# Kernel tuning notes

Measured on AMD Instinct MI355X. Metric: run time of the kernel, lower is better.

The kernel has to match this reference:

```python
import jax, jax.numpy as jnp
import numpy as np

N_NODES = 100000
N_EDGES = 600000
N_GRAPHS = 256
HID = 128
IN_DIM = 7
POCKET_DIM = 28
BN_EPS = 1e-5


def setup_inputs() -> dict:
    key = jax.random.key(0)
    ks = jax.random.split(key, 24)
    d = {}
    d['x'] = jax.random.normal(ks[0], (N_NODES, IN_DIM), dtype=jnp.float32)
    d['edge_index'] = jax.random.randint(ks[1], (2, N_EDGES), 0, N_NODES, dtype=jnp.int32)
    d['batch'] = jnp.sort(jax.random.randint(ks[2], (N_NODES,), 0, N_GRAPHS, dtype=jnp.int32))
    d['pocket'] = jax.random.normal(ks[3], (POCKET_DIM,), dtype=jnp.float32)
    # GCN layer weights (PyG GCNConv: lin then normalized aggregation, bias after)
    def glorot(k, shape):
        lim = np.sqrt(6.0 / (shape[0] + shape[1]))
        return jax.random.uniform(k, shape, jnp.float32, -lim, lim)
    d['W0'] = glorot(ks[4], (IN_DIM, HID)); d['b0'] = jnp.zeros((HID,), jnp.float32)
    d['W1'] = glorot(ks[5], (HID, HID)); d['b1'] = jnp.zeros((HID,), jnp.float32)
    d['W2'] = glorot(ks[6], (HID, HID)); d['b2'] = jnp.zeros((HID,), jnp.float32)
    # BatchNorm (eval mode) params for 3 layers
    d['bn_gamma'] = jax.random.uniform(ks[7], (3, HID), jnp.float32, 0.5, 1.5)
    d['bn_beta'] = 0.1 * jax.random.normal(ks[8], (3, HID), dtype=jnp.float32)
    d['bn_mean'] = 0.1 * jax.random.normal(ks[9], (3, HID), dtype=jnp.float32)
    d['bn_var'] = jax.random.uniform(ks[10], (3, HID), jnp.float32, 0.5, 1.5)
    # pocket MLP: 28 -> 64 -> 64
    d['pw1'] = glorot(ks[11], (POCKET_DIM, 64)); d['pb1'] = jnp.zeros((64,), jnp.float32)
    d['pw2'] = glorot(ks[12], (64, 64)); d['pb2'] = jnp.zeros((64,), jnp.float32)
    # classifier: 192 -> 96 -> 1
    d['cw1'] = glorot(ks[13], (HID + 64, 96)); d['cb1'] = jnp.zeros((96,), jnp.float32)
    d['cw2'] = glorot(ks[14], (96, 1)); d['cb2'] = jnp.zeros((1,), jnp.float32)
    return d


def reference(x, edge_index, batch, pocket, W0, b0, W1, b1, W2, b2,
              bn_gamma, bn_beta, bn_mean, bn_var,
              pw1, pb1, pw2, pb2, cw1, cb1, cw2, cb2):
    src, dst = edge_index[0], edge_index[1]
    n = x.shape[0]
    # degree with self-loops (GCNConv default add_self_loops=True)
    deg = jax.ops.segment_sum(jnp.ones((src.shape[0],), x.dtype), dst, num_segments=n) + 1.0
    dinv = jax.lax.rsqrt(deg)                      # [N]
    norm = dinv[src] * dinv[dst]                   # [E] edge normalization
    self_norm = (dinv * dinv)[:, None]             # [N,1] self-loop norm

    h = x
    for i, (W, b) in enumerate(((W0, b0), (W1, b1), (W2, b2))):
        hl = h @ W                                  # [N,HID]
        agg = jax.ops.segment_sum(hl[src] * norm[:, None], dst, num_segments=n)
        agg = agg + hl * self_norm + b
        # BatchNorm1d in eval mode with running stats
        bn = (agg - bn_mean[i]) * (bn_gamma[i] * jax.lax.rsqrt(bn_var[i] + BN_EPS)) + bn_beta[i]
        h = jax.nn.relu(bn)                         # dropout is identity in eval

    # global mean pool over graphs
    sums = jax.ops.segment_sum(h, batch, num_segments=N_GRAPHS)          # [B,HID]
    cnts = jax.ops.segment_sum(jnp.ones((n,), h.dtype), batch, num_segments=N_GRAPHS)
    lig = sums / jnp.maximum(cnts, 1.0)[:, None]

    # pocket MLP, broadcast to batch
    p = jax.nn.relu(pocket @ pw1 + pb1) @ pw2 + pb2                      # [64]
    pe = jnp.broadcast_to(p[None, :], (N_GRAPHS, 64))

    emb = jnp.concatenate([lig, pe], axis=1)                             # [B,192]
    logits = (jax.nn.relu(emb @ cw1 + cb1) @ cw2 + cb2)[:, 0]            # [B]
    return logits
```

## Files before the change

### kernel.cpp

```cpp
#include <hip/hip_runtime.h>

#define NN 100000
#define NE 600000
#define NG 256
#define HID 128
#define BN_EPS 1e-5f

#define SCAN_TILE 1024
#define NTILES ((NN + SCAN_TILE - 1) / SCAN_TILE)
#define MM_TILES (NN / 32)

typedef __attribute__((ext_vector_type(8))) short short8;
typedef __attribute__((ext_vector_type(4))) float float4v;

__device__ __forceinline__ unsigned short f2bf_rn(float f) {
    unsigned u = __float_as_uint(f);
    unsigned r = u + 0x7FFFu + ((u >> 16) & 1u);
    return (unsigned short)(r >> 16);
}
__device__ __forceinline__ float bf2f(unsigned short h) {
    return __uint_as_float((unsigned)h << 16);
}
__device__ __forceinline__ void unpack8(uint4 u, float* f) {
    f[0] = __uint_as_float(u.x << 16); f[1] = __uint_as_float(u.x & 0xFFFF0000u);
    f[2] = __uint_as_float(u.y << 16); f[3] = __uint_as_float(u.y & 0xFFFF0000u);
    f[4] = __uint_as_float(u.z << 16); f[5] = __uint_as_float(u.z & 0xFFFF0000u);
    f[6] = __uint_as_float(u.w << 16); f[7] = __uint_as_float(u.w & 0xFFFF0000u);
}


__global__ __launch_bounds__(256) void hist_kernel(const int* __restrict__ dst, int* __restrict__ cnt) {
    int e = blockIdx.x * blockDim.x + threadIdx.x;
    if (e < NE) atomicAdd(&cnt[dst[e]], 1);
}


__global__ __launch_bounds__(256) void scan_a(const int* __restrict__ cnt, int* __restrict__ rs,
                                              int* __restrict__ tsum, float* __restrict__ dinv) {
    __shared__ int s[256];
    int t = threadIdx.x;
    int base = blockIdx.x * SCAN_TILE;
    int idx = base + t * 4;
    int v0 = (idx + 0 < NN) ? cnt[idx + 0] : 0;
    int v1 = (idx + 1 < NN) ? cnt[idx + 1] : 0;
    int v2 = (idx + 2 < NN) ? cnt[idx + 2] : 0;
    int v3 = (idx + 3 < NN) ? cnt[idx + 3] : 0;
    if (idx + 0 < NN) dinv[idx + 0] = rsqrtf((float)v0 + 1.0f);
    if (idx + 1 < NN) dinv[idx + 1] = rsqrtf((float)v1 + 1.0f);
    if (idx + 2 < NN) dinv[idx + 2] = rsqrtf((float)v2 + 1.0f);
    if (idx + 3 < NN) dinv[idx + 3] = rsqrtf((float)v3 + 1.0f);
    int local = v0 + v1 + v2 + v3;
    s[t] = local;
    __syncthreads();
    for (int off = 1; off < 256; off <<= 1) {
        int x = (t >= off) ? s[t - off] : 0;
        __syncthreads();
        s[t] += x;
        __syncthreads();
    }
    int pre = s[t] - local;
    if (t == 255) tsum[blockIdx.x] = s[255];
    if (idx + 0 < NN) rs[idx + 0] = pre; pre += v0;
    if (idx + 1 < NN) rs[idx + 1] = pre; pre += v1;
    if (idx + 2 < NN) rs[idx + 2] = pre; pre += v2;
    if (idx + 3 < NN) rs[idx + 3] = pre;
}

__global__ __launch_bounds__(128) void scan_b(int* __restrict__ tsum) {
    __shared__ int s[128];
    int t = threadIdx.x;
    int v = (t < NTILES) ? tsum[t] : 0;
    s[t] = v;
    __syncthreads();
    for (int off = 1; off < 128; off <<= 1) {
        int x = (t >= off) ? s[t - off] : 0;
        __syncthreads();
        s[t] += x;
        __syncthreads();
    }
    if (t < NTILES) tsum[t] = s[t] - v;
}

__global__ __launch_bounds__(256) void scan_c(int* __restrict__ rs, const int* __restrict__ tsum,
                                              int* __restrict__ cursor) {
    int t = threadIdx.x;
    int base = blockIdx.x * SCAN_TILE;
    int off = tsum[blockIdx.x];
    for (int k = 0; k < 4; k++) {
        int idx = base + t * 4 + k;
        if (idx < NN) {
            int v = rs[idx] + off;
            rs[idx] = v;
            cursor[idx] = v;
        }
    }
    if (blockIdx.x == 0 && t == 0) rs[NN] = NE;
}


__global__ __launch_bounds__(256) void bucket_kernel(const int* __restrict__ src, const int* __restrict__ dst,
                                                     int* __restrict__ cursor, int* __restrict__ esrc) {
    int e = blockIdx.x * blockDim.x + threadIdx.x;
    if (e < NE) {
        int pos = atomicAdd(&cursor[dst[e]], 1);
        esrc[pos] = src[e];
    }
}


__global__ __launch_bounds__(256) void prep_kernel(const float* __restrict__ W1, const float* __restrict__ W2,
                                                   unsigned short* __restrict__ w1hi, unsigned short* __restrict__ w1lo,
                                                   unsigned short* __restrict__ w2hi, unsigned short* __restrict__ w2lo,
                                                   const float* __restrict__ pocket,
                                                   const float* __restrict__ pw1, const float* __restrict__ pb1,
                                                   const float* __restrict__ pw2, const float* __restrict__ pb2,
                                                   float* __restrict__ pv) {
    if (blockIdx.x < 64) {
        int t = blockIdx.x * 256 + threadIdx.x;
        int k = t >> 7, n = t & 127;
        int to = n * HID + k;
        float v1 = W1[t];
        unsigned short h1 = f2bf_rn(v1);
        w1hi[to] = h1;
        w1lo[to] = f2bf_rn(v1 - bf2f(h1));
        float v2 = W2[t];
        unsigned short h2 = f2bf_rn(v2);
        w2hi[to] = h2;
        w2lo[to] = f2bf_rn(v2 - bf2f(h2));
    } else {
        __shared__ float t1[64];
        int j = threadIdx.x;
        if (j < 64) {
            float acc = pb1[j];
            for (int k = 0; k < 28; k++) acc = fmaf(pocket[k], pw1[k * 64 + j], acc);
            t1[j] = fmaxf(acc, 0.f);
        }
        __syncthreads();
        if (j < 64) {
            float acc2 = pb2[j];
            for (int k = 0; k < 64; k++) acc2 = fmaf(t1[k], pw2[k * 64 + j], acc2);
            pv[j] = acc2;
        }
    }
}


__global__ __launch_bounds__(256) void xagg_kernel(const float* __restrict__ x,
                                                   const int* __restrict__ rs,
                                                   const int* __restrict__ esrc,
                                                   const float* __restrict__ dinv,
                                                   float* __restrict__ xa) {
    int t = blockIdx.x * blockDim.x + threadIdx.x;
    int f = t & 7;
    int n = t >> 3;
    if (n >= NN) return;
    float acc = 0.f;
    if (f < 7) {
        float di = dinv[n];
        acc = x[n * 7 + f] * di * di;
        int e0 = rs[n], e1 = rs[n + 1];
        int e = e0;
        for (; e + 1 < e1; e += 2) {
            int s0 = esrc[e], s1 = esrc[e + 1];
            float w0 = dinv[s0] * di, w1 = dinv[s1] * di;
            float a0 = x[s0 * 7 + f];
            float a1 = x[s1 * 7 + f];
            acc = fmaf(a0, w0, acc);
            acc = fmaf(a1, w1, acc);
        }
        if (e < e1) {
            int s0 = esrc[e];
            acc = fmaf(x[s0 * 7 + f], dinv[s0] * di, acc);
        }
    }
    xa[n * 8 + f] = acc;
}


__global__ __launch_bounds__(256) void l0_transform(const float* __restrict__ xa,
                                                    const float* __restrict__ W,
                                                    const float* __restrict__ b,
                                                    const float* __restrict__ gamma,
                                                    const float* __restrict__ beta,
                                                    const float* __restrict__ mean,
                                                    const float* __restrict__ var,
                                                    unsigned short* __restrict__ ohi) {
    int c4 = threadIdx.x & 31;
    int r  = threadIdx.x >> 5;
    float w[7][4];
#pragma unroll
    for (int k = 0; k < 7; k++)
#pragma unroll
        for (int i = 0; i < 4; i++) w[k][i] = W[k * HID + c4 * 4 + i];
    float4 bb = ((const float4*)b)[c4];
    float4 ga = ((const float4*)gamma)[c4];
    float4 be = ((const float4*)beta)[c4];
    float4 me = ((const float4*)mean)[c4];
    float4 va = ((const float4*)var)[c4];
    float4 sc;
    sc.x = ga.x * rsqrtf(va.x + BN_EPS);
    sc.y = ga.y * rsqrtf(va.y + BN_EPS);
    sc.z = ga.z * rsqrtf(va.z + BN_EPS);
    sc.w = ga.w * rsqrtf(va.w + BN_EPS);
    __shared__ float s[8][8];
    for (int n0 = blockIdx.x * 8; n0 < NN; n0 += gridDim.x * 8) {
        __syncthreads();
        if (threadIdx.x < 64) s[threadIdx.x >> 3][threadIdx.x & 7] = xa[n0 * 8 + threadIdx.x];
        __syncthreads();
        float o0 = bb.x, o1 = bb.y, o2 = bb.z, o3 = bb.w;
#pragma unroll
        for (int k = 0; k < 7; k++) {
            float xv = s[r][k];
            o0 = fmaf(xv, w[k][0], o0);
            o1 = fmaf(xv, w[k][1], o1);
            o2 = fmaf(xv, w[k][2], o2);
            o3 = fmaf(xv, w[k][3], o3);
        }
        ushort4 hi4;
        hi4.x = f2bf_rn(fmaxf(fmaf(o0 - me.x, sc.x, be.x), 0.f));
        hi4.y = f2bf_rn(fmaxf(fmaf(o1 - me.y, sc.y, be.y), 0.f));
        hi4.z = f2bf_rn(fmaxf(fmaf(o2 - me.z, sc.z, be.z), 0.f));
        hi4.w = f2bf_rn(fmaxf(fmaf(o3 - me.w, sc.w, be.w), 0.f));
        *(ushort4*)(ohi + (size_t)(n0 + r) * HID + c4 * 4) = hi4;
    }
}


__global__ __launch_bounds__(256) void mm_mfma(const unsigned short* __restrict__ A,
                                               const unsigned short* __restrict__ Whi,
                                               const unsigned short* __restrict__ Wlo,
                                               unsigned short* __restrict__ out) {
    int wave = threadIdx.x >> 6;
    int lane = threadIdx.x & 63;
    int mrow = lane & 15;
    int quad = lane >> 4;
    int n0 = wave * 32;

    short8 bh[2][4], bl[2][4];
#pragma unroll
    for (int ct = 0; ct < 2; ct++) {
#pragma unroll
        for (int kc = 0; kc < 4; kc++) {
            size_t off = (size_t)(n0 + ct * 16 + mrow) * HID + kc * 32 + quad * 8;
            bh[ct][kc] = *(const short8*)(Whi + off);
            bl[ct][kc] = *(const short8*)(Wlo + off);
        }
    }

    int tile = blockIdx.x;
    if (tile >= MM_TILES) return;

    short8 ah[2][4];
#pragma unroll
    for (int rt = 0; rt < 2; rt++)
#pragma unroll
        for (int kc = 0; kc < 4; kc++)
            ah[rt][kc] = *(const short8*)(A + (size_t)(tile * 32 + rt * 16 + mrow) * HID + kc * 32 + quad * 8);

    for (;;) {
        int nt = tile + gridDim.x;
        bool has_next = nt < MM_TILES;
        short8 an[2][4];
        if (has_next) {
#pragma unroll
            for (int rt = 0; rt < 2; rt++)
#pragma unroll
                for (int kc = 0; kc < 4; kc++)
                    an[rt][kc] = *(const short8*)(A + (size_t)(nt * 32 + rt * 16 + mrow) * HID + kc * 32 + quad * 8);
        }

        float4v acc[2][2];
#pragma unroll
        for (int rt = 0; rt < 2; rt++)
#pragma unroll
            for (int ct = 0; ct < 2; ct++) {
                acc[rt][ct].x = 0.f; acc[rt][ct].y = 0.f;
                acc[rt][ct].z = 0.f; acc[rt][ct].w = 0.f;
            }

#pragma unroll
        for (int kc = 0; kc < 4; kc++)
#pragma unroll
            for (int rt = 0; rt < 2; rt++)
#pragma unroll
                for (int ct = 0; ct < 2; ct++) {
                    acc[rt][ct] = __builtin_amdgcn_mfma_f32_16x16x32_bf16(ah[rt][kc], bh[ct][kc], acc[rt][ct], 0, 0, 0);
                    acc[rt][ct] = __builtin_amdgcn_mfma_f32_16x16x32_bf16(ah[rt][kc], bl[ct][kc], acc[rt][ct], 0, 0, 0);
                }

        int m0 = tile * 32;
#pragma unroll
        for (int rt = 0; rt < 2; rt++)
#pragma unroll
            for (int ct = 0; ct < 2; ct++) {
                int col = n0 + ct * 16 + mrow;
#pragma unroll
                for (int r = 0; r < 4; r++) {
                    int row = m0 + rt * 16 + quad * 4 + r;
                    out[(size_t)row * HID + col] = f2bf_rn(acc[rt][ct][r]);
                }
            }

        if (!has_next) break;
#pragma unroll
        for (int rt = 0; rt < 2; rt++)
#pragma unroll
            for (int kc = 0; kc < 4; kc++) ah[rt][kc] = an[rt][kc];
        tile = nt;
    }
}


__global__ __launch_bounds__(256) void gather_bn(const unsigned short* __restrict__ hl,
                                                 const int* __restrict__ rs,
                                                 const int* __restrict__ esrc,
                                                 const float* __restrict__ dinv,
                                                 const float* __restrict__ b,
                                                 const float* __restrict__ gamma,
                                                 const float* __restrict__ beta,
                                                 const float* __restrict__ mean,
                                                 const float* __restrict__ var,
                                                 unsigned short* __restrict__ ohi) {
    int t = blockIdx.x * blockDim.x + threadIdx.x;
    int lane = t & 15;
    int n = t >> 4;
    if (n >= NN) return;
    const uint4* hlv = (const uint4*)hl;
    float di = dinv[n];
    float dsq = di * di;

    float acc[8], v[8];
    {
        uint4 sv = hlv[(size_t)n * 16 + lane];
        unpack8(sv, v);
        float4 bA = ((const float4*)b)[lane * 2];
        float4 bB = ((const float4*)b)[lane * 2 + 1];
        acc[0] = fmaf(v[0], dsq, bA.x); acc[1] = fmaf(v[1], dsq, bA.y);
        acc[2] = fmaf(v[2], dsq, bA.z); acc[3] = fmaf(v[3], dsq, bA.w);
        acc[4] = fmaf(v[4], dsq, bB.x); acc[5] = fmaf(v[5], dsq, bB.y);
        acc[6] = fmaf(v[6], dsq, bB.z); acc[7] = fmaf(v[7], dsq, bB.w);
    }

    int e0 = rs[n], e1 = rs[n + 1];
    int e = e0;
    for (; e + 3 < e1; e += 4) {
        int s0 = esrc[e], s1 = esrc[e + 1], s2 = esrc[e + 2], s3 = esrc[e + 3];
        float w0 = dinv[s0] * di, w1 = dinv[s1] * di;
        float w2 = dinv[s2] * di, w3 = dinv[s3] * di;
        uint4 u0 = hlv[(size_t)s0 * 16 + lane];
        uint4 u1 = hlv[(size_t)s1 * 16 + lane];
        uint4 u2 = hlv[(size_t)s2 * 16 + lane];
        uint4 u3 = hlv[(size_t)s3 * 16 + lane];
        unpack8(u0, v);
#pragma unroll
        for (int i = 0; i < 8; i++) acc[i] = fmaf(v[i], w0, acc[i]);
        unpack8(u1, v);
#pragma unroll
        for (int i = 0; i < 8; i++) acc[i] = fmaf(v[i], w1, acc[i]);
        unpack8(u2, v);
#pragma unroll
        for (int i = 0; i < 8; i++) acc[i] = fmaf(v[i], w2, acc[i]);
        unpack8(u3, v);
#pragma unroll
        for (int i = 0; i < 8; i++) acc[i] = fmaf(v[i], w3, acc[i]);
    }
    for (; e < e1; e++) {
        int s0 = esrc[e];
        float w0 = dinv[s0] * di;
        uint4 u0 = hlv[(size_t)s0 * 16 + lane];
        unpack8(u0, v);
#pragma unroll
        for (int i = 0; i < 8; i++) acc[i] = fmaf(v[i], w0, acc[i]);
    }

    float4 gA = ((const float4*)gamma)[lane * 2], gB = ((const float4*)gamma)[lane * 2 + 1];
    float4 eA = ((const float4*)beta)[lane * 2],  eB = ((const float4*)beta)[lane * 2 + 1];
    float4 mA = ((const float4*)mean)[lane * 2],  mB = ((const float4*)mean)[lane * 2 + 1];
    float4 vA = ((const float4*)var)[lane * 2],   vB = ((const float4*)var)[lane * 2 + 1];
    float o[8];
    o[0] = fmaxf(fmaf(acc[0] - mA.x, gA.x * rsqrtf(vA.x + BN_EPS), eA.x), 0.f);
    o[1] = fmaxf(fmaf(acc[1] - mA.y, gA.y * rsqrtf(vA.y + BN_EPS), eA.y), 0.f);
    o[2] = fmaxf(fmaf(acc[2] - mA.z, gA.z * rsqrtf(vA.z + BN_EPS), eA.z), 0.f);
    o[3] = fmaxf(fmaf(acc[3] - mA.w, gA.w * rsqrtf(vA.w + BN_EPS), eA.w), 0.f);
    o[4] = fmaxf(fmaf(acc[4] - mB.x, gB.x * rsqrtf(vB.x + BN_EPS), eB.x), 0.f);
    o[5] = fmaxf(fmaf(acc[5] - mB.y, gB.y * rsqrtf(vB.y + BN_EPS), eB.y), 0.f);
    o[6] = fmaxf(fmaf(acc[6] - mB.z, gB.z * rsqrtf(vB.z + BN_EPS), eB.z), 0.f);
    o[7] = fmaxf(fmaf(acc[7] - mB.w, gB.w * rsqrtf(vB.w + BN_EPS), eB.w), 0.f);

    uint4 p;
    p.x = (unsigned)f2bf_rn(o[0]) | ((unsigned)f2bf_rn(o[1]) << 16);
    p.y = (unsigned)f2bf_rn(o[2]) | ((unsigned)f2bf_rn(o[3]) << 16);
    p.z = (unsigned)f2bf_rn(o[4]) | ((unsigned)f2bf_rn(o[5]) << 16);
    p.w = (unsigned)f2bf_rn(o[6]) | ((unsigned)f2bf_rn(o[7]) << 16);
    ((uint4*)ohi)[(size_t)n * 16 + lane] = p;
}


__global__ __launch_bounds__(1024) void poolcls_kernel(const unsigned short* __restrict__ h,
                                                       const int* __restrict__ batch,
                                                       const float* __restrict__ pv,
                                                       const float* __restrict__ cw1,
                                                       const float* __restrict__ cb1,
                                                       const float* __restrict__ cw2,
                                                       const float* __restrict__ cb2,
                                                       float* __restrict__ out) {
    int g = blockIdx.x;
    int lane = threadIdx.x & 31;
    int row = threadIdx.x >> 5;
    __shared__ int se[2];
    __shared__ float emb[192];
    __shared__ float hid[96];
    if (threadIdx.x < 2) {
        int target = g + threadIdx.x;
        int lo = 0, hi = NN;
        while (lo < hi) {
            int mid = (lo + hi) >> 1;
            if (batch[mid] < target) lo = mid + 1; else hi = mid;
        }
        se[threadIdx.x] = lo;
    }
    if (threadIdx.x < 64) emb[128 + threadIdx.x] = pv[threadIdx.x];
    __syncthreads();
    int start = se[0], end = se[1];
    const uint2* h2 = (const uint2*)h;
    float4 acc = make_float4(0.f, 0.f, 0.f, 0.f);
    for (int n = start + row; n < end; n += 32) {
        uint2 u = h2[(size_t)n * 32 + lane];
        acc.x += __uint_as_float(u.x << 16);
        acc.y += __uint_as_float(u.x & 0xFFFF0000u);
        acc.z += __uint_as_float(u.y << 16);
        acc.w += __uint_as_float(u.y & 0xFFFF0000u);
    }
    __shared__ float4 part[32][32];
    part[row][lane] = acc;
    __syncthreads();
#pragma unroll
    for (int off = 16; off >= 1; off >>= 1) {
        if (row < off) {
            float4 a = part[row][lane];
            float4 c = part[row + off][lane];
            a.x += c.x; a.y += c.y; a.z += c.z; a.w += c.w;
            part[row][lane] = a;
        }
        __syncthreads();
    }
    if (row == 0) {
        float inv = 1.0f / fmaxf((float)(end - start), 1.0f);
        float4 a = part[0][lane];
        a.x *= inv; a.y *= inv; a.z *= inv; a.w *= inv;
        ((float4*)emb)[lane] = a;
    }
    __syncthreads();
    int j = threadIdx.x;
    if (j < 96) {
        float a = cb1[j];
        for (int k = 0; k < 192; k++) a = fmaf(emb[k], cw1[k * 96 + j], a);
        hid[j] = fmaxf(a, 0.f) * cw2[j];
    }
    __syncthreads();
    if (j == 0) {
        float s = cb2[0];
        for (int k = 0; k < 96; k++) s += hid[k];
        out[g] = s;
    }
}

extern "C" void kernel_launch(void* const* d_in, const int* in_sizes, int n_in,
                              void* d_out, int out_size, void* d_ws, size_t ws_size,
                              hipStream_t stream) {
    const float* x        = (const float*)d_in[0];
    const int*   eidx     = (const int*)d_in[1];
    const int*   batch    = (const int*)d_in[2];
    const float* pocket   = (const float*)d_in[3];
    const float* W0 = (const float*)d_in[4];
    const float* b0 = (const float*)d_in[5];
    const float* W1 = (const float*)d_in[6];
    const float* b1 = (const float*)d_in[7];
    const float* W2 = (const float*)d_in[8];
    const float* b2 = (const float*)d_in[9];
    const float* bn_gamma = (const float*)d_in[10];
    const float* bn_beta  = (const float*)d_in[11];
    const float* bn_mean  = (const float*)d_in[12];
    const float* bn_var   = (const float*)d_in[13];
    const float* pw1 = (const float*)d_in[14]; const float* pb1 = (const float*)d_in[15];
    const float* pw2 = (const float*)d_in[16]; const float* pb2 = (const float*)d_in[17];
    const float* cw1 = (const float*)d_in[18]; const float* cb1 = (const float*)d_in[19];
    const float* cw2 = (const float*)d_in[20]; const float* cb2 = (const float*)d_in[21];
    float* out = (float*)d_out;

    float* ws   = (float*)d_ws;
    float* dinv = ws;
    int*   cnt  = (int*)(ws + NN);
    int*   rs   = cnt + NN;
    int*   tsum = rs + NN + 1;
    int*   esrc = tsum + 128;
    float* xa   = (float*)(esrc + NE);
    unsigned short* w1hi = (unsigned short*)(xa + (size_t)NN * 8);
    unsigned short* w1lo = w1hi + HID * HID;
    unsigned short* w2hi = w1lo + HID * HID;
    unsigned short* w2lo = w2hi + HID * HID;
    size_t head = (size_t)NN * 2 + (NN + 1) + 128 + NE + (size_t)NN * 8
                + (4 * HID * HID) / 2;
    head = (head + 3) & ~(size_t)3;
    unsigned short* A = (unsigned short*)(ws + head);
    unsigned short* B = A + (size_t)NN * HID;
    float* pv   = (float*)(B + (size_t)NN * HID);

    const int* srcp = eidx;
    const int* dstp = eidx + NE;

    hipMemsetAsync(cnt, 0, NN * sizeof(int), stream);
    hist_kernel<<<(NE + 255) / 256, 256, 0, stream>>>(dstp, cnt);
    scan_a<<<NTILES, 256, 0, stream>>>(cnt, rs, tsum, dinv);
    scan_b<<<1, 128, 0, stream>>>(tsum);
    scan_c<<<NTILES, 256, 0, stream>>>(rs, tsum, cnt);
    bucket_kernel<<<(NE + 255) / 256, 256, 0, stream>>>(srcp, dstp, cnt, esrc);
    prep_kernel<<<65, 256, 0, stream>>>(W1, W2, w1hi, w1lo, w2hi, w2lo,
                                        pocket, pw1, pb1, pw2, pb2, pv);

    xagg_kernel<<<(NN * 8 + 255) / 256, 256, 0, stream>>>(x, rs, esrc, dinv, xa);
    l0_transform<<<2048, 256, 0, stream>>>(xa, W0, b0,
                                           bn_gamma + 0 * HID, bn_beta + 0 * HID,
                                           bn_mean + 0 * HID, bn_var + 0 * HID, A);

    const int MM_BLOCKS = 1024;
    const int GA_BLOCKS = (NN * 16 + 255) / 256;

    mm_mfma<<<MM_BLOCKS, 256, 0, stream>>>(A, w1hi, w1lo, B);
    gather_bn<<<GA_BLOCKS, 256, 0, stream>>>(
        B, rs, esrc, dinv, b1,
        bn_gamma + 1 * HID, bn_beta + 1 * HID, bn_mean + 1 * HID, bn_var + 1 * HID, A);
    mm_mfma<<<MM_BLOCKS, 256, 0, stream>>>(A, w2hi, w2lo, B);
    gather_bn<<<GA_BLOCKS, 256, 0, stream>>>(
        B, rs, esrc, dinv, b2,
        bn_gamma + 2 * HID, bn_beta + 2 * HID, bn_mean + 2 * HID, bn_var + 2 * HID, A);

    poolcls_kernel<<<NG, 1024, 0, stream>>>(A, batch, pv, cw1, cb1, cw2, cb2, out);
}
```

Measured before the change: 340.7 us.

## Fuse bucket with weight prep and layer-0 aggregation with transform; resize mm grid

Merges the edge-bucketing kernel and the weight/pocket prep kernel into one launch by splitting on block index. Fuses the layer-0 feature aggregation into the layer-0 linear+BN transform, so the 8-wide intermediate xa is kept in shared memory instead of being written to and read back from global memory, and that buffer is removed from the workspace. The mm_mfma grid changes from 1024 blocks to half the number of 32-row tiles. The aim is fewer launches and less global traffic; the fused kernel runs the irregular gather inside a block that also does the transform, which can reduce latency hiding.

```diff
diff --git a/kernel.cpp b/kernel.cpp
--- a/kernel.cpp
+++ b/kernel.cpp
@@ -98,25 +98,23 @@
 }
 
 
-__global__ __launch_bounds__(256) void bucket_kernel(const int* __restrict__ src, const int* __restrict__ dst,
-                                                     int* __restrict__ cursor, int* __restrict__ esrc) {
-    int e = blockIdx.x * blockDim.x + threadIdx.x;
-    if (e < NE) {
-        int pos = atomicAdd(&cursor[dst[e]], 1);
-        esrc[pos] = src[e];
-    }
-}
-
-
-__global__ __launch_bounds__(256) void prep_kernel(const float* __restrict__ W1, const float* __restrict__ W2,
-                                                   unsigned short* __restrict__ w1hi, unsigned short* __restrict__ w1lo,
-                                                   unsigned short* __restrict__ w2hi, unsigned short* __restrict__ w2lo,
-                                                   const float* __restrict__ pocket,
-                                                   const float* __restrict__ pw1, const float* __restrict__ pb1,
-                                                   const float* __restrict__ pw2, const float* __restrict__ pb2,
-                                                   float* __restrict__ pv) {
-    if (blockIdx.x < 64) {
-        int t = blockIdx.x * 256 + threadIdx.x;
+__global__ __launch_bounds__(256) void bucket_prep_kernel(const int* __restrict__ src, const int* __restrict__ dst,
+                                                          int* __restrict__ cursor, int* __restrict__ esrc,
+                                                          const float* __restrict__ W1, const float* __restrict__ W2,
+                                                          unsigned short* __restrict__ w1hi, unsigned short* __restrict__ w1lo,
+                                                          unsigned short* __restrict__ w2hi, unsigned short* __restrict__ w2lo,
+                                                          const float* __restrict__ pocket,
+                                                          const float* __restrict__ pw1, const float* __restrict__ pb1,
+                                                          const float* __restrict__ pw2, const float* __restrict__ pb2,
+                                                          float* __restrict__ pv, int nb) {
+    if ((int)blockIdx.x < nb) {
+        int e = blockIdx.x * 256 + threadIdx.x;
+        if (e < NE) {
+            int pos = atomicAdd(&cursor[dst[e]], 1);
+            esrc[pos] = src[e];
+        }
+    } else if ((int)blockIdx.x < nb + 64) {
+        int t = (blockIdx.x - nb) * 256 + threadIdx.x;
         int k = t >> 7, n = t & 127;
         int to = n * HID + k;
         float v1 = W1[t];
@@ -145,48 +143,19 @@
 }
 
 
-__global__ __launch_bounds__(256) void xagg_kernel(const float* __restrict__ x,
-                                                   const int* __restrict__ rs,
-                                                   const int* __restrict__ esrc,
-                                                   const float* __restrict__ dinv,
-                                                   float* __restrict__ xa) {
-    int t = blockIdx.x * blockDim.x + threadIdx.x;
-    int f = t & 7;
-    int n = t >> 3;
-    if (n >= NN) return;
-    float acc = 0.f;
-    if (f < 7) {
-        float di = dinv[n];
-        acc = x[n * 7 + f] * di * di;
-        int e0 = rs[n], e1 = rs[n + 1];
-        int e = e0;
-        for (; e + 1 < e1; e += 2) {
-            int s0 = esrc[e], s1 = esrc[e + 1];
-            float w0 = dinv[s0] * di, w1 = dinv[s1] * di;
-            float a0 = x[s0 * 7 + f];
-            float a1 = x[s1 * 7 + f];
-            acc = fmaf(a0, w0, acc);
-            acc = fmaf(a1, w1, acc);
-        }
-        if (e < e1) {
-            int s0 = esrc[e];
-            acc = fmaf(x[s0 * 7 + f], dinv[s0] * di, acc);
-        }
-    }
-    xa[n * 8 + f] = acc;
-}
-
-
-__global__ __launch_bounds__(256) void l0_transform(const float* __restrict__ xa,
-                                                    const float* __restrict__ W,
-                                                    const float* __restrict__ b,
-                                                    const float* __restrict__ gamma,
-                                                    const float* __restrict__ beta,
-                                                    const float* __restrict__ mean,
-                                                    const float* __restrict__ var,
-                                                    unsigned short* __restrict__ ohi) {
+__global__ __launch_bounds__(256) void l0_fused(const float* __restrict__ x,
+                                                const int* __restrict__ rs,
+                                                const int* __restrict__ esrc,
+                                                const float* __restrict__ dinv,
+                                                const float* __restrict__ W,
+                                                const float* __restrict__ b,
+                                                const float* __restrict__ gamma,
+                                                const float* __restrict__ beta,
+                                                const float* __restrict__ mean,
+                                                const float* __restrict__ var,
+                                                unsigned short* __restrict__ ohi) {
     int c4 = threadIdx.x & 31;
-    int r  = threadIdx.x >> 5;
+    int r8 = threadIdx.x >> 5;
     float w[7][4];
 #pragma unroll
     for (int k = 0; k < 7; k++)
@@ -202,26 +171,51 @@
     sc.y = ga.y * rsqrtf(va.y + BN_EPS);
     sc.z = ga.z * rsqrtf(va.z + BN_EPS);
     sc.w = ga.w * rsqrtf(va.w + BN_EPS);
-    __shared__ float s[8][8];
-    for (int n0 = blockIdx.x * 8; n0 < NN; n0 += gridDim.x * 8) {
-        __syncthreads();
-        if (threadIdx.x < 64) s[threadIdx.x >> 3][threadIdx.x & 7] = xa[n0 * 8 + threadIdx.x];
-        __syncthreads();
-        float o0 = bb.x, o1 = bb.y, o2 = bb.z, o3 = bb.w;
-#pragma unroll
-        for (int k = 0; k < 7; k++) {
-            float xv = s[r][k];
-            o0 = fmaf(xv, w[k][0], o0);
-            o1 = fmaf(xv, w[k][1], o1);
-            o2 = fmaf(xv, w[k][2], o2);
-            o3 = fmaf(xv, w[k][3], o3);
-        }
-        ushort4 hi4;
-        hi4.x = f2bf_rn(fmaxf(fmaf(o0 - me.x, sc.x, be.x), 0.f));
-        hi4.y = f2bf_rn(fmaxf(fmaf(o1 - me.y, sc.y, be.y), 0.f));
-        hi4.z = f2bf_rn(fmaxf(fmaf(o2 - me.z, sc.z, be.z), 0.f));
-        hi4.w = f2bf_rn(fmaxf(fmaf(o3 - me.w, sc.w, be.w), 0.f));
-        *(ushort4*)(ohi + (size_t)(n0 + r) * HID + c4 * 4) = hi4;
+    int m = threadIdx.x >> 3, f = threadIdx.x & 7;
+    __shared__ float s[32][8];
+    for (int n0 = blockIdx.x * 32; n0 < NN; n0 += gridDim.x * 32) {
+        __syncthreads();
+        float acc = 0.f;
+        int n = n0 + m;
+        if (f < 7) {
+            float di = dinv[n];
+            acc = x[n * 7 + f] * di * di;
+            int e0 = rs[n], e1 = rs[n + 1];
+            int e = e0;
+            for (; e + 1 < e1; e += 2) {
+                int s0 = esrc[e], s1 = esrc[e + 1];
+                float w0 = dinv[s0] * di, w1 = dinv[s1] * di;
+                float a0 = x[s0 * 7 + f];
+                float a1 = x[s1 * 7 + f];
+                acc = fmaf(a0, w0, acc);
+                acc = fmaf(a1, w1, acc);
+            }
+            if (e < e1) {
+                int s0 = esrc[e];
+                acc = fmaf(x[s0 * 7 + f], dinv[s0] * di, acc);
+            }
+        }
+        s[m][f] = acc;
+        __syncthreads();
+#pragma unroll
+        for (int g = 0; g < 4; g++) {
+            int m2 = g * 8 + r8;
+            float o0 = bb.x, o1 = bb.y, o2 = bb.z, o3 = bb.w;
+#pragma unroll
+            for (int k = 0; k < 7; k++) {
+                float xv = s[m2][k];
+                o0 = fmaf(xv, w[k][0], o0);
+                o1 = fmaf(xv, w[k][1], o1);
+                o2 = fmaf(xv, w[k][2], o2);
+                o3 = fmaf(xv, w[k][3], o3);
+            }
+            ushort4 hi4;
+            hi4.x = f2bf_rn(fmaxf(fmaf(o0 - me.x, sc.x, be.x), 0.f));
+            hi4.y = f2bf_rn(fmaxf(fmaf(o1 - me.y, sc.y, be.y), 0.f));
+            hi4.z = f2bf_rn(fmaxf(fmaf(o2 - me.z, sc.z, be.z), 0.f));
+            hi4.w = f2bf_rn(fmaxf(fmaf(o3 - me.w, sc.w, be.w), 0.f));
+            *(ushort4*)(ohi + (size_t)(n0 + m2) * HID + c4 * 4) = hi4;
+        }
     }
 }
 
@@ -494,13 +488,11 @@
     int*   rs   = cnt + NN;
     int*   tsum = rs + NN + 1;
     int*   esrc = tsum + 128;
-    float* xa   = (float*)(esrc + NE);
-    unsigned short* w1hi = (unsigned short*)(xa + (size_t)NN * 8);
+    unsigned short* w1hi = (unsigned short*)(esrc + NE);
     unsigned short* w1lo = w1hi + HID * HID;
     unsigned short* w2hi = w1lo + HID * HID;
     unsigned short* w2lo = w2hi + HID * HID;
-    size_t head = (size_t)NN * 2 + (NN + 1) + 128 + NE + (size_t)NN * 8
-                + (4 * HID * HID) / 2;
+    size_t head = (size_t)NN * 2 + (NN + 1) + 128 + NE + (4 * HID * HID) / 2;
     head = (head + 3) & ~(size_t)3;
     unsigned short* A = (unsigned short*)(ws + head);
     unsigned short* B = A + (size_t)NN * HID;
@@ -509,21 +501,22 @@
     const int* srcp = eidx;
     const int* dstp = eidx + NE;
 
+    const int NB = (NE + 255) / 256;
+
     hipMemsetAsync(cnt, 0, NN * sizeof(int), stream);
-    hist_kernel<<<(NE + 255) / 256, 256, 0, stream>>>(dstp, cnt);
+    hist_kernel<<<NB, 256, 0, stream>>>(dstp, cnt);
     scan_a<<<NTILES, 256, 0, stream>>>(cnt, rs, tsum, dinv);
     scan_b<<<1, 128, 0, stream>>>(tsum);
     scan_c<<<NTILES, 256, 0, stream>>>(rs, tsum, cnt);
-    bucket_kernel<<<(NE + 255) / 256, 256, 0, stream>>>(srcp, dstp, cnt, esrc);
-    prep_kernel<<<65, 256, 0, stream>>>(W1, W2, w1hi, w1lo, w2hi, w2lo,
-                                        pocket, pw1, pb1, pw2, pb2, pv);
-
-    xagg_kernel<<<(NN * 8 + 255) / 256, 256, 0, stream>>>(x, rs, esrc, dinv, xa);
-    l0_transform<<<2048, 256, 0, stream>>>(xa, W0, b0,
-                                           bn_gamma + 0 * HID, bn_beta + 0 * HID,
-                                           bn_mean + 0 * HID, bn_var + 0 * HID, A);
-
-    const int MM_BLOCKS = 1024;
+    bucket_prep_kernel<<<NB + 65, 256, 0, stream>>>(srcp, dstp, cnt, esrc,
+                                                    W1, W2, w1hi, w1lo, w2hi, w2lo,
+                                                    pocket, pw1, pb1, pw2, pb2, pv, NB);
+
+    l0_fused<<<1024, 256, 0, stream>>>(x, rs, esrc, dinv, W0, b0,
+                                       bn_gamma + 0 * HID, bn_beta + 0 * HID,
+                                       bn_mean + 0 * HID, bn_var + 0 * HID, A);
+
+    const int MM_BLOCKS = (MM_TILES + 1) / 2;
     const int GA_BLOCKS = (NN * 16 + 255) / 256;
 
     mm_mfma<<<MM_BLOCKS, 256, 0, stream>>>(A, w1hi, w1lo, B);
```

Measured after the change: 347.9 us. +2.1%, slower.
